# Kernel tuning notes

Measured on AMD Instinct MI355X. Metric: run time of the kernel, lower is better.

## Reference

```python
import jax, jax.numpy as jnp
import numpy as np

H = 8        # num_heads
HKV = 4      # kv_heads
WINDOW = 12  # sliding-window size (Chebyshev distance on the 2D grid)
BASE = 10000.0


def _rope_tables(N, head_dim, base=BASE):
    """2D axial RoPE for a square grid: first half of head_dim -> H pos, second -> W pos."""
    side = int(round(N ** 0.5))
    assert side * side == N
    dq = head_dim // 4
    inv = 1.0 / (base ** (np.arange(dq, dtype=np.float32) / dq))
    gh, gw = np.meshgrid(np.arange(side, dtype=np.float32), np.arange(side, dtype=np.float32), indexing='ij')
    th = np.outer(gh.ravel(), inv)   # [N, dq]
    tw = np.outer(gw.ravel(), inv)   # [N, dq]
    theta = np.concatenate([th, tw], axis=1)        # [N, head_dim//2]
    theta = np.concatenate([theta, theta], axis=1)  # [N, head_dim]
    return jnp.asarray(np.cos(theta)), jnp.asarray(np.sin(theta))


def _window_mask(N, window):
    """Additive mask: -inf where Chebyshev distance on the sqrt(N) x sqrt(N) grid > window."""
    side = int(round(N ** 0.5))
    idx = np.arange(side)
    gh, gw = np.meshgrid(idx, idx, indexing='ij')
    coords = np.stack([gh.ravel(), gw.ravel()], axis=1)            # [N, 2]
    dist = np.abs(coords[:, None, :] - coords[None, :, :]).max(-1)  # [N, N]
    return jnp.asarray(np.where(dist > window, -np.inf, 0.0).astype(np.float32))


def _rotate_half(x):
    x1, x2 = jnp.split(x, 2, axis=-1)
    return jnp.concatenate([-x2, x1], axis=-1)


def _apply_rope(x, cos, sin):
    # x: [B,H,N,d]; cos/sin: [N,d] broadcast over batch/heads
    return x * cos + _rotate_half(x) * sin


def _l2norm(x, eps=1e-12):
    return x / jnp.sqrt(jnp.sum(x * x, axis=-1, keepdims=True) + eps)


def setup_inputs() -> dict:
    key = jax.random.key(0)
    ks = jax.random.split(key, 7)
    B, N, C = 4, 2304, 512
    x = jax.random.normal(ks[0], (B, N, C), dtype=jnp.float32)
    Wq = jax.random.normal(ks[1], (C, 2 * C), dtype=jnp.float32) * 0.02
    Wk = jax.random.normal(ks[2], (C, 2 * C * HKV // H), dtype=jnp.float32) * 0.02
    Wv1 = jax.random.normal(ks[3], (C, C * HKV // H), dtype=jnp.float32) * 0.02
    Wv2 = jax.random.normal(ks[4], (C, C * HKV // H), dtype=jnp.float32) * 0.02
    lambda_p = jnp.full((H, 1, 1), -2.0, dtype=jnp.float32)
    Wp = jax.random.normal(ks[5], (C, C), dtype=jnp.float32) * 0.02
    bp = jnp.zeros((C,), dtype=jnp.float32)
    return {"x": x, "Wq": Wq, "Wk": Wk, "Wv1": Wv1, "Wv2": Wv2,
            "lambda_p": lambda_p, "Wp": Wp, "bp": bp}


def reference(x, Wq, Wk, Wv1, Wv2, lambda_p, Wp, bp):
    B, N, C = x.shape
    d = C // H
    scale = d ** -0.5
    cos, sin = _rope_tables(N, d)
    mask = _window_mask(N, WINDOW)  # [N,N] additive

    def to_heads(t, h):  # [B,N,h*d] -> [B,h,N,d]
        return t.reshape(B, N, h, -1).transpose(0, 2, 1, 3)

    q = x @ Wq                                  # [B,N,2C]
    q1, q2 = jnp.split(q, 2, axis=-1)
    q1, q2 = to_heads(q1, H), to_heads(q2, H)   # [B,H,N,d]
    k = x @ Wk                                  # [B,N,2*C*HKV/H]
    k1, k2 = jnp.split(k, 2, axis=-1)
    k1, k2 = to_heads(k1, HKV), to_heads(k2, HKV)  # [B,HKV,N,d]
    v1 = to_heads(x @ Wv1, HKV)
    v2 = to_heads(x @ Wv2, HKV)

    # QK-norm (L2) then RoPE
    q1, q2, k1, k2 = (_l2norm(t) for t in (q1, q2, k1, k2))
    q1 = _apply_rope(q1, cos, sin)
    q2 = _apply_rope(q2, cos, sin)
    k1 = _apply_rope(k1, cos, sin)
    k2 = _apply_rope(k2, cos, sin)

    # GQA: repeat KV heads to match query heads
    rep = H // HKV
    k1, k2 = jnp.repeat(k1, rep, axis=1), jnp.repeat(k2, rep, axis=1)
    v1, v2 = jnp.repeat(v1, rep, axis=1), jnp.repeat(v2, rep, axis=1)

    attn1 = jax.nn.softmax(jnp.einsum('bhnd,bhmd->bhnm', q1, k1) * scale + mask, axis=-1)
    attn2 = jax.nn.softmax(jnp.einsum('bhnd,bhmd->bhnm', q2, k2) * scale + mask, axis=-1)
    lam = jax.nn.sigmoid(lambda_p)[None]  # [1,H,1,1]
    out = jnp.einsum('bhnm,bhmd->bhnd', attn1, v1) - lam * jnp.einsum('bhnm,bhmd->bhnd', attn2, v2)
    out = out.transpose(0, 2, 1, 3).reshape(B, N, C)
    return out @ Wp + bp
```

## Files before the change

kernel.cpp:

```cpp
#include <hip/hip_runtime.h>
#include <stdint.h>

typedef unsigned short u16;
typedef __attribute__((ext_vector_type(8))) short bf16x8;
typedef __attribute__((ext_vector_type(4))) float f32x4;

#define LOG2E 1.4426950408889634f
#define QSCALE (0.125f * LOG2E)

__device__ __forceinline__ float bf2f(u16 u) {
    union { uint32_t i; float f; } v; v.i = ((uint32_t)u) << 16; return v.f;
}
__device__ __forceinline__ u16 f2bf(float f) {
    union { float f; uint32_t i; } v; v.f = f;
    uint32_t i = v.i;
    return (u16)((i + 0x7FFF + ((i >> 16) & 1)) >> 16);
}
__device__ __forceinline__ uint32_t cvt_pk_bf16(float a, float b) {
    uint32_t r;
    asm("v_cvt_pk_bf16_f32 %0, %1, %2" : "=v"(r) : "v"(a), "v"(b));
    return r;
}
__device__ __forceinline__ int imin(int a, int b) { return a < b ? a : b; }
__device__ __forceinline__ int imax(int a, int b) { return a > b ? a : b; }

__device__ __forceinline__ void gl_lds16(const void* g, void* l) {
    __builtin_amdgcn_global_load_lds(
        (const __attribute__((address_space(1))) uint32_t*)g,
        (__attribute__((address_space(3))) uint32_t*)l, 16, 0, 0);
}

__device__ __forceinline__ float exp2q(float t) {
    const float a = 0.6946474805f;
    const float b = 0.2402265069f;
    return fmaf(fmaf(b, t, a), t, 1.0f);
}

union U8 { bf16x8 v; uint32_t u[4]; };

__global__ void k_prep(const float* __restrict__ x,
                       const float* __restrict__ Wq, const float* __restrict__ Wk,
                       const float* __restrict__ Wv1, const float* __restrict__ Wv2,
                       const float* __restrict__ Wp,
                       float* __restrict__ tab, u16* __restrict__ xb,
                       u16* __restrict__ WCT, u16* __restrict__ WPT) {
    __shared__ u16 tile[64][65];
    int bid = blockIdx.x;
    if (bid < 288) {
        int t = bid * 256 + threadIdx.x;
        if (t >= 2304 * 32) return;
        int n = t >> 5, j = t & 31;
        int gh = n / 48, gw = n % 48;
        float f = (float)(j & 15);
        float coord = (j < 16) ? (float)gh : (float)gw;
        float inv = exp2f(-f * (13.287712379549449f / 16.0f));
        float th = coord * inv;
        tab[t * 2 + 0] = cosf(th);
        tab[t * 2 + 1] = sinf(th);
    } else if (bid < 4896) {
        int t = (bid - 288) * 256 + threadIdx.x;
        if (t >= 9216 * 512 / 4) return;
        float4 v = ((const float4*)x)[t];
        ushort4 o;
        o.x = f2bf(v.x); o.y = f2bf(v.y); o.z = f2bf(v.z); o.w = f2bf(v.w);
        ((ushort4*)xb)[t] = o;
    } else {
        int jb = bid - 4896;
        int n0 = (jb % 40) * 64;
        int k0 = (jb / 40) * 64;
        int c = threadIdx.x & 63;
        int rr = threadIdx.x >> 6;
        const float* src; int stride; int roff; u16* dst; int nb;
        if (n0 < 1024)      { src = Wq;  stride = 1024; roff = 0;    dst = WCT; nb = n0; }
        else if (n0 < 1536) { src = Wk;  stride = 512;  roff = 1024; dst = WCT; nb = n0; }
        else if (n0 < 1792) { src = Wv1; stride = 256;  roff = 1536; dst = WCT; nb = n0; }
        else if (n0 < 2048) { src = Wv2; stride = 256;  roff = 1792; dst = WCT; nb = n0; }
        else                { src = Wp;  stride = 512;  roff = 2048; dst = WPT; nb = n0 - 2048; }
        int scol = n0 + c - roff;
#pragma unroll
        for (int i = 0; i < 16; ++i) {
            int k = rr * 16 + i;
            tile[c][k] = f2bf(src[(size_t)(k0 + k) * stride + scol]);
        }
        __syncthreads();
        int kk = threadIdx.x & 63;
        int c4 = threadIdx.x >> 6;
#pragma unroll
        for (int i = 0; i < 16; ++i) {
            int nl = c4 * 16 + i;
            dst[(size_t)(nb + nl) * 512 + k0 + kk] = tile[nl][kk];
        }
    }
}

__global__ __launch_bounds__(256) void k_gemm_qkv(
    const u16* __restrict__ A, const u16* __restrict__ BT,
    const float* __restrict__ tab,
    u16* __restrict__ Q1, u16* __restrict__ Q2,
    u16* __restrict__ KF1, u16* __restrict__ KF2,
    u16* __restrict__ VF1, u16* __restrict__ VF2) {
    __shared__ u16 Asw[128 * 64];
    __shared__ u16 Bsw[128 * 64];
    const int K = 512;
    int id = blockIdx.x + 16 * blockIdx.y;
    int l = (id & 7) * 144 + (id >> 3);
    int n0 = (l & 15) * 128;
    int m0 = (l >> 4) * 128;
    int tid = threadIdx.x;
    int lane = tid & 63, w = tid >> 6;
    int wm = w >> 1, wn = w & 1;
    int li = lane & 15, g = lane >> 4;
    f32x4 zero4 = {0.f, 0.f, 0.f, 0.f};
    f32x4 acc[4][4];
#pragma unroll
    for (int mi = 0; mi < 4; ++mi)
#pragma unroll
        for (int ni = 0; ni < 4; ++ni) acc[mi][ni] = zero4;

    for (int k0 = 0; k0 < K; k0 += 64) {
        __syncthreads();
#pragma unroll
        for (int p = 0; p < 4; ++p) {
            int cidx = p * 256 + tid;
            int r = cidx >> 3, j = cidx & 7;
            int jj = j ^ (r & 7);
            gl_lds16(A  + (size_t)(m0 + r) * K + k0 + jj * 8, (char*)Asw + cidx * 16);
            gl_lds16(BT + (size_t)(n0 + r) * K + k0 + jj * 8, (char*)Bsw + cidx * 16);
        }
        __syncthreads();
#pragma unroll
        for (int ks = 0; ks < 2; ++ks) {
            bf16x8 af[4], bfr[4];
#pragma unroll
            for (int mi = 0; mi < 4; ++mi) {
                int r = wm * 64 + mi * 16 + li;
                int kc = ks * 4 + g;
                af[mi] = *(const bf16x8*)((const char*)Asw + r * 128 + ((kc ^ (r & 7)) * 16));
            }
#pragma unroll
            for (int ni = 0; ni < 4; ++ni) {
                int r = wn * 64 + ni * 16 + li;
                int kc = ks * 4 + g;
                bfr[ni] = *(const bf16x8*)((const char*)Bsw + r * 128 + ((kc ^ (r & 7)) * 16));
            }
#pragma unroll
            for (int mi = 0; mi < 4; ++mi)
#pragma unroll
                for (int ni = 0; ni < 4; ++ni)
                    acc[mi][ni] = __builtin_amdgcn_mfma_f32_16x16x32_bf16(af[mi], bfr[ni], acc[mi][ni], 0, 0, 0);
        }
    }

    int colbase = n0 + wn * 64;
    int b = m0 / 2304;
    int nbase = (m0 % 2304) + wm * 64;

    if (colbase < 1536) {
        u16* out; int isK; size_t hb;
        if (colbase < 1024) {
            out = (colbase < 512) ? Q1 : Q2;
            int h = (colbase >> 6) & 7;
            hb = (size_t)(b * 8 + h) * 2304;
            isK = 0;
        } else {
            out = (colbase < 1280) ? KF1 : KF2;
            int hkv = ((colbase - 1024) >> 6) & 3;
            hb = (size_t)(b * 4 + hkv) * 48;
            isK = 1;
        }
        float qs = isK ? 1.0f : QSCALE;
#pragma unroll
        for (int mi = 0; mi < 4; ++mi) {
            float rsq[4];
#pragma unroll
            for (int r = 0; r < 4; ++r) {
                float ss = 0.f;
#pragma unroll
                for (int ni = 0; ni < 4; ++ni) ss += acc[mi][ni][r] * acc[mi][ni][r];
                ss += __shfl_xor(ss, 1, 64);
                ss += __shfl_xor(ss, 2, 64);
                ss += __shfl_xor(ss, 4, 64);
                ss += __shfl_xor(ss, 8, 64);
                rsq[r] = qs / sqrtf(ss + 1e-12f);
            }
#pragma unroll
            for (int r = 0; r < 4; ++r) {
                int n = nbase + mi * 16 + g * 4 + r;
                float2 cs0 = *(const float2*)(tab + ((size_t)n * 32 + li) * 2);
                float2 cs1 = *(const float2*)(tab + ((size_t)n * 32 + 16 + li) * 2);
                float y[4];
#pragma unroll
                for (int ni = 0; ni < 4; ++ni) {
                    float c = (ni & 1) ? cs1.x : cs0.x;
                    float s = (ni & 1) ? cs1.y : cs0.y;
                    float p = acc[mi][ni ^ 2][r];
                    float t = (ni < 2) ? (acc[mi][ni][r] * c - p * s)
                                       : (acc[mi][ni][r] * c + p * s);
                    y[ni] = t * rsq[r];
                }
                if (!isK) {
                    size_t obase = (hb + n) * 64;
#pragma unroll
                    for (int ni = 0; ni < 4; ++ni)
                        out[obase + ni * 16 + li] = f2bf(y[ni]);
                } else {
                    int kh = n / 48, r48 = n % 48;
                    int kt = r48 >> 4, lq = r48 & 15;
                    size_t base = (hb + kh) * 3072;
#pragma unroll
                    for (int ni = 0; ni < 4; ++ni) {
                        int sC = ni >> 1;
                        int gg = ((ni & 1) << 1) + (li >> 3);
                        int e = li & 7;
                        out[base + (size_t)(((kt * 2 + sC) * 64 + gg * 16 + lq) * 8 + e)] = f2bf(y[ni]);
                    }
                }
            }
        }
    } else {
        u16* out = (colbase < 1792) ? VF1 : VF2;
        int hkv = ((colbase - 1536) >> 6) & 3;
        size_t hb = (size_t)(b * 4 + hkv) * 48;
#pragma unroll
        for (int mi = 0; mi < 4; ++mi) {
            int n4 = nbase + mi * 16 + g * 4;
            int kh = n4 / 48, r48 = n4 % 48;
            int grp = r48 >> 2;
            int kt = grp >> 2, gp = grp & 3;
            size_t base = (hb + kh) * 3072;
#pragma unroll
            for (int ni = 0; ni < 4; ++ni) {
                uint2 val;
                val.x = cvt_pk_bf16(acc[mi][ni][0], acc[mi][ni][1]);
                val.y = cvt_pk_bf16(acc[mi][ni][2], acc[mi][ni][3]);
                *(uint2*)(out + base + (size_t)(((ni * 3 + kt) * 64 + gp * 16 + li) * 4)) = val;
            }
        }
    }
}

__global__ __launch_bounds__(256) void k_gemm_o64(
    const u16* __restrict__ A, const u16* __restrict__ BT,
    float* __restrict__ Cout, const float* __restrict__ bias) {
    __shared__ u16 Asw[64 * 64];
    __shared__ u16 Bsw[64 * 64];
    const int K = 512;
    const int N = 512;
    int id = blockIdx.x + 8 * blockIdx.y;
    int l = (id & 7) * 144 + (id >> 3);
    int n0 = (l & 7) * 64;
    int m0 = (l >> 3) * 64;
    int tid = threadIdx.x;
    int lane = tid & 63, w = tid >> 6;
    int wm = w >> 1, wn = w & 1;
    int li = lane & 15, g = lane >> 4;
    f32x4 zero4 = {0.f, 0.f, 0.f, 0.f};
    f32x4 acc[2][2];
#pragma unroll
    for (int mi = 0; mi < 2; ++mi)
#pragma unroll
        for (int ni = 0; ni < 2; ++ni) acc[mi][ni] = zero4;

    for (int k0 = 0; k0 < K; k0 += 64) {
        __syncthreads();
#pragma unroll
        for (int p = 0; p < 2; ++p) {
            int ci = p * 256 + tid;
            int r = ci >> 3, j = ci & 7;
            int jj = j ^ (r & 7);
            gl_lds16(A  + (size_t)(m0 + r) * K + k0 + jj * 8, (char*)Asw + ci * 16);
            gl_lds16(BT + (size_t)(n0 + r) * K + k0 + jj * 8, (char*)Bsw + ci * 16);
        }
        __syncthreads();
#pragma unroll
        for (int ks = 0; ks < 2; ++ks) {
            bf16x8 af[2], bfr[2];
#pragma unroll
            for (int mi = 0; mi < 2; ++mi) {
                int r = wm * 32 + mi * 16 + li;
                int kc = ks * 4 + g;
                af[mi] = *(const bf16x8*)((const char*)Asw + r * 128 + ((kc ^ (r & 7)) * 16));
            }
#pragma unroll
            for (int ni = 0; ni < 2; ++ni) {
                int r = wn * 32 + ni * 16 + li;
                int kc = ks * 4 + g;
                bfr[ni] = *(const bf16x8*)((const char*)Bsw + r * 128 + ((kc ^ (r & 7)) * 16));
            }
#pragma unroll
            for (int mi = 0; mi < 2; ++mi)
#pragma unroll
                for (int ni = 0; ni < 2; ++ni)
                    acc[mi][ni] = __builtin_amdgcn_mfma_f32_16x16x32_bf16(af[mi], bfr[ni], acc[mi][ni], 0, 0, 0);
        }
    }
#pragma unroll
    for (int mi = 0; mi < 2; ++mi)
#pragma unroll
        for (int ni = 0; ni < 2; ++ni) {
#pragma unroll
            for (int r = 0; r < 4; ++r) {
                int row = m0 + wm * 32 + mi * 16 + g * 4 + r;
                int col = n0 + wn * 32 + ni * 16 + li;
                Cout[(size_t)row * N + col] = acc[mi][ni][r] + bias[col];
            }
        }
}

template <int A, int NTT>
__device__ __forceinline__ void load_k(const u16* __restrict__ kb, bf16x8 (&kf)[NTT][2], int lane) {
#pragma unroll
    for (int t = 0; t < NTT; ++t)
#pragma unroll
        for (int s = 0; s < 2; ++s)
            kf[t][s] = *(const bf16x8*)(kb + ((A + t) * 2 + s) * 512 + lane * 8);
}

template <int A, int NTT>
__device__ __forceinline__ void load_v(const u16* __restrict__ vb, uint2 (&ch)[4][NTT], int lane) {
#pragma unroll
    for (int dt = 0; dt < 4; ++dt)
#pragma unroll
        for (int t = 0; t < NTT; ++t)
            ch[dt][t] = *(const uint2*)(vb + ((dt * 3 + A + t) * 64 + lane) * 4);
}

template <int A, int NTT>
__device__ __forceinline__ void attn_core(
    const bf16x8 (&kf)[NTT][2], const uint2 (&ch)[4][NTT],
    const bf16x8 (&qf)[2][2], const float (&bmul)[3][4],
    f32x4 (&Oa)[2][4], float (&sum)[2]) {
    __builtin_amdgcn_s_setprio(1);
    U8 pa0[2], pa1[2];
#pragma unroll
    for (int h = 0; h < 2; ++h) {
        f32x4 S[NTT];
#pragma unroll
        for (int t = 0; t < NTT; ++t) {
            f32x4 z = {0.f, 0.f, 0.f, 0.f};
            z = __builtin_amdgcn_mfma_f32_16x16x32_bf16(kf[t][0], qf[h][0], z, 0, 0, 0);
            S[t] = __builtin_amdgcn_mfma_f32_16x16x32_bf16(kf[t][1], qf[h][1], z, 0, 0, 0);
        }
        uint32_t pk[NTT][2];
#pragma unroll
        for (int t = 0; t < NTT; ++t)
#pragma unroll
            for (int rp = 0; rp < 2; ++rp) {
                float p0 = exp2q(S[t][2 * rp])     * bmul[A + t][2 * rp];
                float p1 = exp2q(S[t][2 * rp + 1]) * bmul[A + t][2 * rp + 1];
                sum[h] += p0 + p1;
                pk[t][rp] = cvt_pk_bf16(p0, p1);
            }
        pa0[h].u[0] = pk[0][0]; pa0[h].u[1] = pk[0][1];
        pa0[h].u[2] = pk[1][0]; pa0[h].u[3] = pk[1][1];
        if (NTT == 3) { pa1[h].u[0] = pk[2][0]; pa1[h].u[1] = pk[2][1]; pa1[h].u[2] = 0; pa1[h].u[3] = 0; }
    }
#pragma unroll
    for (int dt = 0; dt < 4; ++dt) {
        union { bf16x8 v; uint2 q[2]; } vf0, vf1;
        vf0.q[0] = ch[dt][0]; vf0.q[1] = ch[dt][1];
        if (NTT == 3) { vf1.q[0] = ch[dt][2]; vf1.q[1] = ch[dt][2]; }
#pragma unroll
        for (int h = 0; h < 2; ++h) {
            Oa[h][dt] = __builtin_amdgcn_mfma_f32_16x16x32_bf16(pa0[h].v, vf0.v, Oa[h][dt], 0, 0, 0);
            if (NTT == 3)
                Oa[h][dt] = __builtin_amdgcn_mfma_f32_16x16x32_bf16(pa1[h].v, vf1.v, Oa[h][dt], 0, 0, 0);
        }
    }
    __builtin_amdgcn_s_setprio(0);
}

template <int A, int NTT>
__device__ __forceinline__ void attn_step_local(
    const bf16x8 (&kf)[NTT][2], const u16* __restrict__ vb,
    const bf16x8 (&qf)[2][2], const float (&bmul)[3][4],
    f32x4 (&Oa)[2][4], float (&sum)[2], int lane) {
    uint2 ch[4][NTT];
    load_v<A, NTT>(vb, ch, lane);
    attn_core<A, NTT>(kf, ch, qf, bmul, Oa, sum);
}

template <int A, int NTT>
__device__ __forceinline__ void run_range(
    const u16* __restrict__ kp, const u16* __restrict__ vp, int n,
    const bf16x8 (&qf)[2][2], const float (&bmul)[3][4],
    f32x4 (&Oa)[2][4], float (&sum)[2], int lane) {
    bf16x8 kA[NTT][2], kB[NTT][2];
    load_k<A, NTT>(kp, kA, lane);
    int i = 0;
    for (; i + 2 <= n; i += 2) {
        load_k<A, NTT>(kp + 3072, kB, lane);
        attn_step_local<A, NTT>(kA, vp, qf, bmul, Oa, sum, lane);
        load_k<A, NTT>(kp + ((i + 3 <= n) ? 6144 : 3072), kA, lane);
        attn_step_local<A, NTT>(kB, vp + 3072, qf, bmul, Oa, sum, lane);
        kp += 6144; vp += 6144;
    }
    if (i < n) attn_step_local<A, NTT>(kA, vp, qf, bmul, Oa, sum, lane);
}

template <int A>
__device__ __forceinline__ void run_range_pf(
    const u16* __restrict__ kp, const u16* __restrict__ vp, int n,
    const bf16x8 (&qf)[2][2], const float (&bmul)[3][4],
    f32x4 (&Oa)[2][4], float (&sum)[2], int lane) {
    bf16x8 kA[2][2], kB[2][2];
    uint2 vA[4][2], vB[4][2];
    load_k<A, 2>(kp, kA, lane);
    load_v<A, 2>(vp, vA, lane);
    int i = 0;
    for (; i + 2 <= n; i += 2) {
        load_k<A, 2>(kp + 3072, kB, lane);
        load_v<A, 2>(vp + 3072, vB, lane);
        attn_core<A, 2>(kA, vA, qf, bmul, Oa, sum);
        int adv = (i + 3 <= n) ? 6144 : 3072;
        load_k<A, 2>(kp + adv, kA, lane);
        load_v<A, 2>(vp + adv, vA, lane);
        attn_core<A, 2>(kB, vB, qf, bmul, Oa, sum);
        kp += 6144; vp += 6144;
    }
    if (i < n) attn_core<A, 2>(kA, vA, qf, bmul, Oa, sum);
}

__global__ __launch_bounds__(128) void k_attention(
    const u16* __restrict__ Q1, const u16* __restrict__ Q2,
    const u16* __restrict__ KF1, const u16* __restrict__ KF2,
    const u16* __restrict__ VF1, const u16* __restrict__ VF2,
    const float* __restrict__ lambda_p, u16* __restrict__ AOUT) {
    __shared__ float obuf[2][16][64];
    int tid = threadIdx.x;
    int lane = tid & 63, beta = tid >> 6;
    int li = lane & 15, g = lane >> 4;
    int hw = blockIdx.x;
    int l = (hw & 7) * 288 + (hw >> 3);
    int mu = l % 3, j = (l / 3) % 48, kvb = l / 144;
    int m2 = j >> 1;
    int qh = (j & 1) ? (23 - m2) : (24 + m2);
    int hkv = kvb & 3, b = kvb >> 2;

    const u16* Qb = beta ? Q2 : Q1;

    bf16x8 qf[2][2];
#pragma unroll
    for (int h2 = 0; h2 < 2; ++h2)
#pragma unroll
        for (int s = 0; s < 2; ++s)
            qf[h2][s] = *(const bf16x8*)(Qb + ((size_t)(b * 8 + hkv * 2 + h2) * 2304
                            + qh * 48 + mu * 16 + li) * 64 + s * 32 + g * 8);

    float bmul[3][4];
    int qw = mu * 16 + li;
#pragma unroll
    for (int t = 0; t < 3; ++t)
#pragma unroll
        for (int r = 0; r < 4; ++r) {
            int kw = t * 16 + 4 * g + r;
            int dw = qw - kw; if (dw < 0) dw = -dw;
            bmul[t][r] = (dw <= 12) ? 1.0f : 0.0f;
        }

    f32x4 zero4 = {0.f, 0.f, 0.f, 0.f};
    f32x4 Oa[2][4];
#pragma unroll
    for (int h = 0; h < 2; ++h)
#pragma unroll
        for (int dt = 0; dt < 4; ++dt) Oa[h][dt] = zero4;
    float sum[2] = {0.f, 0.f};

    int kh0 = imax(0, qh - 12), kh1 = imin(47, qh + 12);
    int niter = kh1 - kh0 + 1;
    const u16* kp = (beta ? KF2 : KF1) + ((size_t)kvb * 48 + kh0) * 3072;
    const u16* vp = (beta ? VF2 : VF1) + ((size_t)kvb * 48 + kh0) * 3072;

    if (mu == 1)      run_range<0, 3>(kp, vp, niter, qf, bmul, Oa, sum, lane);
    else if (mu == 0) run_range_pf<0>(kp, vp, niter, qf, bmul, Oa, sum, lane);
    else              run_range_pf<1>(kp, vp, niter, qf, bmul, Oa, sum, lane);

    float inv[2][4];
#pragma unroll
    for (int h = 0; h < 2; ++h) {
        float s = sum[h];
        s += __shfl_xor(s, 16, 64);
        s += __shfl_xor(s, 32, 64);
#pragma unroll
        for (int r = 0; r < 4; ++r)
            inv[h][r] = 1.0f / __shfl(s, 4 * g + r, 64);
    }

    if (beta == 1) {
#pragma unroll
        for (int h = 0; h < 2; ++h)
#pragma unroll
            for (int dt = 0; dt < 4; ++dt)
#pragma unroll
                for (int r = 0; r < 4; ++r)
                    obuf[h][4 * g + r][dt * 16 + li] = Oa[h][dt][r] * inv[h][r];
    }
    __syncthreads();
    if (beta == 0) {
#pragma unroll
        for (int h = 0; h < 2; ++h) {
            float lam = 1.0f / (1.0f + expf(-lambda_p[hkv * 2 + h]));
#pragma unroll
            for (int dt = 0; dt < 4; ++dt)
#pragma unroll
                for (int r = 0; r < 4; ++r) {
                    float o1 = Oa[h][dt][r] * inv[h][r];
                    float o2 = obuf[h][4 * g + r][dt * 16 + li];
                    int n = qh * 48 + mu * 16 + 4 * g + r;
                    int colc = (hkv * 2 + h) * 64 + dt * 16 + li;
                    AOUT[((size_t)(b * 2304 + n)) * 512 + colc] = f2bf(o1 - lam * o2);
                }
        }
    }
}

extern "C" void kernel_launch(void* const* d_in, const int* in_sizes, int n_in,
                              void* d_out, int out_size, void* d_ws, size_t ws_size,
                              hipStream_t stream) {
    const float* x        = (const float*)d_in[0];
    const float* Wq       = (const float*)d_in[1];
    const float* Wk       = (const float*)d_in[2];
    const float* Wv1      = (const float*)d_in[3];
    const float* Wv2      = (const float*)d_in[4];
    const float* lambda_p = (const float*)d_in[5];
    const float* Wp       = (const float*)d_in[6];
    const float* bp       = (const float*)d_in[7];

    char* ws = (char*)d_ws;
    size_t off = 0;
    auto alloc = [&](size_t bytes) { char* p = ws + off; off += (bytes + 255) & ~(size_t)255; return p; };
    float* rope = (float*)alloc((size_t)2304 * 32 * 2 * 4);
    u16* XB     = (u16*)alloc((size_t)9216 * 512 * 2);
    u16* WCT    = (u16*)alloc((size_t)2048 * 512 * 2);
    u16* WPT    = (u16*)alloc((size_t)512 * 512 * 2);
    u16* Q1     = (u16*)alloc((size_t)4 * 8 * 2304 * 64 * 2);
    u16* Q2     = (u16*)alloc((size_t)4 * 8 * 2304 * 64 * 2);
    u16* KF1    = (u16*)alloc((size_t)16 * 48 * 3072 * 2);
    u16* KF2    = (u16*)alloc((size_t)16 * 48 * 3072 * 2);
    u16* VF1    = (u16*)alloc((size_t)16 * 48 * 3072 * 2);
    u16* VF2    = (u16*)alloc((size_t)16 * 48 * 3072 * 2);
    u16* AOUT   = (u16*)alloc((size_t)9216 * 512 * 2);

    k_prep<<<5216, 256, 0, stream>>>(x, Wq, Wk, Wv1, Wv2, Wp, rope, XB, WCT, WPT);
    k_gemm_qkv<<<dim3(16, 72), 256, 0, stream>>>(XB, WCT, rope, Q1, Q2, KF1, KF2, VF1, VF2);
    k_attention<<<2304, 128, 0, stream>>>(Q1, Q2, KF1, KF2, VF1, VF2, lambda_p, AOUT);
    k_gemm_o64<<<dim3(8, 144), 256, 0, stream>>>(AOUT, WPT, (float*)d_out, bp);
}
```

Measured before the change: 120.3 us.

## Replace double-buffered K/V prefetch loops with simple loop and raise occupancy

Removes the software double-buffering of K and V fragments in the attention loop, so each iteration loads its K/V tile and computes on it right away. It also adds a minimum-blocks-per-SM hint of 5 to launch_bounds. Register pressure drops, so more waves can be resident and hide memory latency instead of explicit prefetch. The risk is exposed load latency per iteration if occupancy does not rise enough, or spills forced by the bound.

```diff
diff --git a/kernel.cpp b/kernel.cpp
--- a/kernel.cpp
+++ b/kernel.cpp
@@ -371,57 +371,21 @@
 }
 
 template <int A, int NTT>
-__device__ __forceinline__ void attn_step_local(
-    const bf16x8 (&kf)[NTT][2], const u16* __restrict__ vb,
-    const bf16x8 (&qf)[2][2], const float (&bmul)[3][4],
-    f32x4 (&Oa)[2][4], float (&sum)[2], int lane) {
-    uint2 ch[4][NTT];
-    load_v<A, NTT>(vb, ch, lane);
-    attn_core<A, NTT>(kf, ch, qf, bmul, Oa, sum);
-}
-
-template <int A, int NTT>
-__device__ __forceinline__ void run_range(
+__device__ __forceinline__ void run_simple(
     const u16* __restrict__ kp, const u16* __restrict__ vp, int n,
     const bf16x8 (&qf)[2][2], const float (&bmul)[3][4],
     f32x4 (&Oa)[2][4], float (&sum)[2], int lane) {
-    bf16x8 kA[NTT][2], kB[NTT][2];
-    load_k<A, NTT>(kp, kA, lane);
-    int i = 0;
-    for (; i + 2 <= n; i += 2) {
-        load_k<A, NTT>(kp + 3072, kB, lane);
-        attn_step_local<A, NTT>(kA, vp, qf, bmul, Oa, sum, lane);
-        load_k<A, NTT>(kp + ((i + 3 <= n) ? 6144 : 3072), kA, lane);
-        attn_step_local<A, NTT>(kB, vp + 3072, qf, bmul, Oa, sum, lane);
-        kp += 6144; vp += 6144;
-    }
-    if (i < n) attn_step_local<A, NTT>(kA, vp, qf, bmul, Oa, sum, lane);
-}
-
-template <int A>
-__device__ __forceinline__ void run_range_pf(
-    const u16* __restrict__ kp, const u16* __restrict__ vp, int n,
-    const bf16x8 (&qf)[2][2], const float (&bmul)[3][4],
-    f32x4 (&Oa)[2][4], float (&sum)[2], int lane) {
-    bf16x8 kA[2][2], kB[2][2];
-    uint2 vA[4][2], vB[4][2];
-    load_k<A, 2>(kp, kA, lane);
-    load_v<A, 2>(vp, vA, lane);
-    int i = 0;
-    for (; i + 2 <= n; i += 2) {
-        load_k<A, 2>(kp + 3072, kB, lane);
-        load_v<A, 2>(vp + 3072, vB, lane);
-        attn_core<A, 2>(kA, vA, qf, bmul, Oa, sum);
-        int adv = (i + 3 <= n) ? 6144 : 3072;
-        load_k<A, 2>(kp + adv, kA, lane);
-        load_v<A, 2>(vp + adv, vA, lane);
-        attn_core<A, 2>(kB, vB, qf, bmul, Oa, sum);
-        kp += 6144; vp += 6144;
-    }
-    if (i < n) attn_core<A, 2>(kA, vA, qf, bmul, Oa, sum);
-}
-
-__global__ __launch_bounds__(128) void k_attention(
+    for (int i = 0; i < n; ++i) {
+        bf16x8 kf[NTT][2];
+        uint2 ch[4][NTT];
+        load_k<A, NTT>(kp, kf, lane);
+        load_v<A, NTT>(vp, ch, lane);
+        attn_core<A, NTT>(kf, ch, qf, bmul, Oa, sum);
+        kp += 3072; vp += 3072;
+    }
+}
+
+__global__ __launch_bounds__(128, 5) void k_attention(
     const u16* __restrict__ Q1, const u16* __restrict__ Q2,
     const u16* __restrict__ KF1, const u16* __restrict__ KF2,
     const u16* __restrict__ VF1, const u16* __restrict__ VF2,
@@ -471,9 +435,9 @@
     const u16* kp = (beta ? KF2 : KF1) + ((size_t)kvb * 48 + kh0) * 3072;
     const u16* vp = (beta ? VF2 : VF1) + ((size_t)kvb * 48 + kh0) * 3072;
 
-    if (mu == 1)      run_range<0, 3>(kp, vp, niter, qf, bmul, Oa, sum, lane);
-    else if (mu == 0) run_range_pf<0>(kp, vp, niter, qf, bmul, Oa, sum, lane);
-    else              run_range_pf<1>(kp, vp, niter, qf, bmul, Oa, sum, lane);
+    if (mu == 1)      run_simple<0, 3>(kp, vp, niter, qf, bmul, Oa, sum, lane);
+    else if (mu == 0) run_simple<0, 2>(kp, vp, niter, qf, bmul, Oa, sum, lane);
+    else              run_simple<1, 2>(kp, vp, niter, qf, bmul, Oa, sum, lane);
 
     float inv[2][4];
 #pragma unroll
```

Measured after the change: 236.4 us. +96.4%, slower.
